# Optimization experiments

Hardware: AMD Instinct MI355X
Metric: run time of the kernel (lower is better)

Reference implementation:

```python
import jax, jax.numpy as jnp
import numpy as np

FEAT_STRIDE = 16
PRE_NMS = 6000   # TEST config
POST_NMS = 300
NMS_TH = 0.7


def _generate_anchors_3d(base_size=16, ratios=(0.5, 1.0, 2.0), scales=(8, 16, 32), time_dims=(16,)):
    """Standard Faster-RCNN anchor enumeration, extended with a time extent.
    Returns (A, 6) float32 boxes in [x1, y1, z1, x2, y2, z2] order (matches shift order)."""
    w = h = float(base_size)
    xc = yc = 0.5 * (base_size - 1)
    size = w * h
    ratios = np.asarray(ratios, dtype=np.float64)
    ws = np.round(np.sqrt(size / ratios))
    hs = np.round(ws * ratios)
    a2 = []
    for wi, hi in zip(ws, hs):
        for s in scales:
            ww, hh = wi * s, hi * s
            a2.append([xc - 0.5 * (ww - 1), yc - 0.5 * (hh - 1),
                       xc + 0.5 * (ww - 1), yc + 0.5 * (hh - 1)])
    out = []
    for t in time_dims:
        for a in a2:
            out.append([a[0], a[1], 0.0, a[2], a[3], float(t) - 1.0])
    return np.asarray(out, dtype=np.float32)


def setup_inputs() -> dict:
    key = jax.random.key(0)
    k1, k2 = jax.random.split(key)
    B, A, H, W, T = 2, 9, 32, 32, 16
    scores_map = jax.random.normal(k1, (B, 2 * A, H, W, T), dtype=jnp.float32)
    bbox_frame = jax.random.normal(k2, (B, 6 * A, H, W, T), dtype=jnp.float32) * 0.2
    im_info = jnp.array([512.0, 512.0, 16.0], dtype=jnp.float32)  # [img_h, img_w, n_frames]
    anchors = jnp.asarray(_generate_anchors_3d())  # (9, 6)
    return {"scores_map": scores_map, "bbox_frame": bbox_frame, "im_info": im_info, "anchors": anchors}


def _nms_single(boxes, scs):
    """Greedy 3D (spatio-temporal volume) NMS for one image.
    boxes: (N, 6), scs: (N,). Returns (POST_NMS, 7) rows [score, x1,y1,z1,x2,y2,z2],
    zero-padded past the number of kept proposals (matches output[i].zero_() + fill)."""
    order = jnp.argsort(-scs)[:PRE_NMS]           # descending score, pre-NMS top-k
    b = boxes[order]                              # (P, 6)
    s = scs[order]                                # (P,)
    vol = (b[:, 3] - b[:, 0] + 1.0) * (b[:, 4] - b[:, 1] + 1.0) * (b[:, 5] - b[:, 2] + 1.0)
    iw = jnp.clip(jnp.minimum(b[:, None, 3], b[None, :, 3]) - jnp.maximum(b[:, None, 0], b[None, :, 0]) + 1.0, 0.0)
    ih = jnp.clip(jnp.minimum(b[:, None, 4], b[None, :, 4]) - jnp.maximum(b[:, None, 1], b[None, :, 1]) + 1.0, 0.0)
    il = jnp.clip(jnp.minimum(b[:, None, 5], b[None, :, 5]) - jnp.maximum(b[:, None, 2], b[None, :, 2]) + 1.0, 0.0)
    inter = iw * ih * il                          # (P, P)
    iou = inter / (vol[:, None] + vol[None, :] - inter)
    iou = jax.lax.stop_gradient(iou)              # keep mask is non-differentiable
    P = b.shape[0]
    idx = jnp.arange(P)

    def step(keep, i):
        sup = (iou[i] > NMS_TH) & keep[i] & (idx > i)
        return keep & ~sup, None

    keep, _ = jax.lax.scan(step, jnp.ones((P,), dtype=bool), jnp.arange(P))
    rank = jnp.cumsum(keep) - 1
    pos = jnp.where(keep & (rank < POST_NMS), rank, POST_NMS)  # overflow slot POST_NMS
    rows = jnp.concatenate([s[:, None], b], axis=1)            # (P, 7)
    out = jnp.zeros((POST_NMS + 1, 7), dtype=boxes.dtype).at[pos].set(rows)
    return out[:POST_NMS]


def reference(scores_map, bbox_frame, im_info, anchors):
    A = anchors.shape[0]
    B = scores_map.shape[0]
    scores = scores_map[:, A:]                    # (B, A, H, W, T) foreground scores
    H, W, T = scores.shape[2], scores.shape[3], scores.shape[4]

    # --- anchor grid (matches np.meshgrid 'xy' + ravel = H-major, W, T order) ---
    sx = (jnp.arange(W) * FEAT_STRIDE).astype(scores_map.dtype)
    sy = (jnp.arange(H) * FEAT_STRIDE).astype(scores_map.dtype)
    sz = jnp.arange(T).astype(scores_map.dtype)
    X, Y, Z = jnp.meshgrid(sx, sy, sz)            # each (H, W, T)
    shift = jnp.stack([X.ravel(), Y.ravel(), Z.ravel()], axis=1)   # (K, 3)
    shifts = jnp.concatenate([shift, shift], axis=1)               # (K, 6)
    all_anchors = (anchors[None] + shifts[:, None]).reshape(-1, 6)  # (K*A, 6)

    deltas = bbox_frame.transpose(0, 2, 3, 4, 1).reshape(B, -1, 6)  # (B, K*A, 6)
    scs = scores.transpose(0, 2, 3, 4, 1).reshape(B, -1)            # (B, K*A)

    # --- bbox_transform_inv_3d ---
    aw = all_anchors[:, 3] - all_anchors[:, 0] + 1.0
    ah = all_anchors[:, 4] - all_anchors[:, 1] + 1.0
    al = all_anchors[:, 5] - all_anchors[:, 2] + 1.0
    acx = all_anchors[:, 0] + 0.5 * aw
    acy = all_anchors[:, 1] + 0.5 * ah
    acz = all_anchors[:, 2] + 0.5 * al
    pcx = deltas[..., 0] * aw + acx
    pcy = deltas[..., 1] * ah + acy
    pcz = deltas[..., 2] * al + acz
    pw = jnp.exp(deltas[..., 3]) * aw
    ph = jnp.exp(deltas[..., 4]) * ah
    pl = jnp.exp(deltas[..., 5]) * al
    proposals = jnp.stack([pcx - 0.5 * pw, pcy - 0.5 * ph, pcz - 0.5 * pl,
                           pcx + 0.5 * pw, pcy + 0.5 * ph, pcz + 0.5 * pl], axis=-1)

    # --- clip_boxes_3d: x in [0, img_w-1], y in [0, img_h-1], z in [0, n_frames-1] ---
    lim = jnp.stack([im_info[1], im_info[0], im_info[2],
                     im_info[1], im_info[0], im_info[2]]) - 1.0
    proposals = jnp.clip(proposals, 0.0, lim)

    return jax.vmap(_nms_single)(proposals, scs)  # (B, POST_NMS, 7)
```

## Files before the change

kernel.cpp:

```cpp
#include <hip/hip_runtime.h>
#include <stdint.h>

#define FEAT_STRIDE 16
#define PRE_NMS 6000
#define POST_NMS 300
#define NMS_TH 0.7f

static constexpr int B_ = 2, A_ = 9, H_ = 32, W_ = 32, T_ = 16;
static constexpr int LOC = H_ * W_ * T_;
static constexpr int N_ = LOC * A_;
static constexpr int NBIN = 65536;
static constexpr int NREP = 8;
static constexpr int CAP = 8192;
static constexpr int NW = 94;
static constexpr int ROWS = 6016;

static constexpr double BMID = 0.7000000178813934326171875;


__device__ __forceinline__ uint32_t f2u(float f) {
    uint32_t b = __float_as_uint(f);
    return b ^ ((b >> 31) ? 0xFFFFFFFFu : 0x80000000u);
}
__device__ __forceinline__ float u2f(uint32_t u) {
    uint32_t b = (u >> 31) ? (u ^ 0x80000000u) : ~u;
    return __uint_as_float(b);
}
__device__ __forceinline__ unsigned long long rl64(unsigned long long v, int lane) {
    unsigned int lo = (unsigned int)__builtin_amdgcn_readlane((int)(unsigned int)v, lane);
    unsigned int hi = (unsigned int)__builtin_amdgcn_readlane((int)(unsigned int)(v >> 32), lane);
    return ((unsigned long long)hi << 32) | lo;
}

__global__ void hist_kernel(const float* __restrict__ scores_map,
                            unsigned int* __restrict__ histR) {
    int gid = blockIdx.x * blockDim.x + threadIdx.x;
    if (gid >= B_ * N_) return;
    int b = gid / N_;
    int r = gid - b * N_;
    int a = r / LOC;
    int loc = r - a * LOC;
    float sc = scores_map[((size_t)(b * 2 * A_ + A_ + a)) * LOC + loc];
    uint32_t u = f2u(sc);
    int rep = blockIdx.x & (NREP - 1);
    atomicAdd(&histR[((size_t)(rep * B_ + b)) * NBIN + (u >> 16)], 1u);
}

__global__ void __launch_bounds__(256) partial_kernel(
        const unsigned int* __restrict__ histR,
        unsigned int* __restrict__ partials) {
    int c = blockIdx.x, bb = blockIdx.y, t = threadIdx.x;
    unsigned int s = 0;
#pragma unroll
    for (int r = 0; r < NREP; ++r) {
        const uint4* h4 = reinterpret_cast<const uint4*>(
            histR + ((size_t)(r * B_ + bb)) * NBIN + c * 1024);
        uint4 v = h4[t];
        s += v.x + v.y + v.z + v.w;
    }
    __shared__ unsigned int red[256];
    red[t] = s;
    __syncthreads();
    for (int off = 128; off > 0; off >>= 1) {
        if (t < off) red[t] += red[t + off];
        __syncthreads();
    }
    if (t == 0) partials[bb * 64 + c] = red[0];
}

__global__ void __launch_bounds__(256) rewrite_kernel(
        const unsigned int* __restrict__ histR,
        unsigned int* __restrict__ hist,
        unsigned int* __restrict__ binbase,
        const unsigned int* __restrict__ partials,
        unsigned int* __restrict__ thr) {
    int c = blockIdx.x, bb = blockIdx.y, t = threadIdx.x;
    __shared__ unsigned int sp[64];
    __shared__ unsigned int ssum[256];
    if (t < 64) sp[t] = partials[bb * 64 + t];
    uint4 v = {0u, 0u, 0u, 0u};
#pragma unroll
    for (int r = 0; r < NREP; ++r) {
        const uint4* h4 = reinterpret_cast<const uint4*>(
            histR + ((size_t)(r * B_ + bb)) * NBIN + c * 1024);
        uint4 w = h4[t];
        v.x += w.x; v.y += w.y; v.z += w.z; v.w += w.w;
    }
    unsigned int* h = hist + (size_t)bb * NBIN + c * 1024;
    unsigned int* bs = binbase + (size_t)bb * NBIN + c * 1024;
    ssum[t] = v.x + v.y + v.z + v.w;
    __syncthreads();
    unsigned int chunkBase = 0;
    for (int q = c + 1; q < 64; ++q) chunkBase += sp[q];
    for (int off = 1; off < 256; off <<= 1) {
        unsigned int val = (t + off < 256) ? ssum[t + off] : 0u;
        __syncthreads();
        ssum[t] += val;
        __syncthreads();
    }
    unsigned int run = chunkBase + ((t < 255) ? ssum[t + 1] : 0u);
    unsigned int cnt[4] = {v.x, v.y, v.z, v.w};
    unsigned int offv[4];
    for (int q = 3; q >= 0; --q) {
        offv[q] = run;
        unsigned int newrun = run + cnt[q];
        if (run < (unsigned)PRE_NMS && newrun >= (unsigned)PRE_NMS) {
            thr[bb * 2 + 0] = (unsigned)(c * 1024 + t * 4 + q);
            thr[bb * 2 + 1] = newrun;
        }
        run = newrun;
    }
    uint4 o4 = {offv[0], offv[1], offv[2], offv[3]};
    reinterpret_cast<uint4*>(h)[t] = o4;
    reinterpret_cast<uint4*>(bs)[t] = o4;
}

__global__ void __launch_bounds__(256) compact_kernel(
        const float* __restrict__ scores_map,
        const unsigned int* __restrict__ thr,
        unsigned long long* __restrict__ cand,
        unsigned int* __restrict__ hist) {
    int tid = threadIdx.x;
    int gid = blockIdx.x * 256 + tid;
    int b = gid / N_;
    int r = gid - b * N_;
    int a = r / LOC;
    int loc = r - a * LOC;
    float sc = scores_map[((size_t)(b * 2 * A_ + A_ + a)) * LOC + loc];
    uint32_t u = f2u(sc);
    uint32_t bin = u >> 16;
    if (bin >= thr[b * 2]) {
        int n = loc * A_ + a;
        unsigned long long key = ((unsigned long long)u << 18)
                               | (unsigned long long)(N_ - 1 - n);
        unsigned int slot = atomicAdd(&hist[b * NBIN + bin], 1u);
        if (slot < (unsigned)CAP)
            cand[(size_t)b * CAP + slot] = key;
    }
}

__global__ void __launch_bounds__(256) bucket_decode(
        const unsigned long long* __restrict__ cand,
        const unsigned int* __restrict__ hist,
        const unsigned int* __restrict__ binbase,
        const unsigned int* __restrict__ thr,
        const float* __restrict__ bbox_frame,
        const float* __restrict__ im_info,
        const float* __restrict__ anchors,
        float* __restrict__ sortedBox) {
    int gid = blockIdx.x * 256 + threadIdx.x;
    int bb = gid / CAP;
    int i = gid - bb * CAP;
    int count = (int)thr[bb * 2 + 1];
    if (count > CAP) count = CAP;
    if (i >= count) return;
    const unsigned long long* cb = cand + (size_t)bb * CAP;
    unsigned long long me = cb[i];
    int bin = (int)(me >> 34);
    int start = (int)binbase[bb * NBIN + bin];
    int end = (int)hist[bb * NBIN + bin];
    if (end > count) end = count;
    int rank = start;
    for (int q = start; q < end; ++q)
        rank += (cb[q] > me);
    if (rank >= PRE_NMS) return;

    uint32_t u = (uint32_t)(me >> 18);
    int n = N_ - 1 - (int)(me & 0x3FFFFull);
    int a = n % A_;
    int loc = n / A_;
    int k = loc % T_;
    int j = (loc / T_) % W_;
    int ii = loc / (T_ * W_);

    float ax1 = anchors[a * 6 + 0] + (float)(FEAT_STRIDE * j);
    float ay1 = anchors[a * 6 + 1] + (float)(FEAT_STRIDE * ii);
    float az1 = anchors[a * 6 + 2] + (float)k;
    float ax2 = anchors[a * 6 + 3] + (float)(FEAT_STRIDE * j);
    float ay2 = anchors[a * 6 + 4] + (float)(FEAT_STRIDE * ii);
    float az2 = anchors[a * 6 + 5] + (float)k;
    float aw = ax2 - ax1 + 1.0f, ah = ay2 - ay1 + 1.0f, al = az2 - az1 + 1.0f;
    float acx = ax1 + 0.5f * aw, acy = ay1 + 0.5f * ah, acz = az1 + 0.5f * al;

    const float* dp = bbox_frame + ((size_t)(bb * 6 * A_ + a * 6)) * LOC
                    + ii * (W_ * T_) + j * T_ + k;
    float d0 = dp[0 * LOC], d1 = dp[1 * LOC], d2 = dp[2 * LOC];
    float d3 = dp[3 * LOC], d4 = dp[4 * LOC], d5 = dp[5 * LOC];

    float pcx = d0 * aw + acx, pcy = d1 * ah + acy, pcz = d2 * al + acz;
    float pw = expf(d3) * aw, ph = expf(d4) * ah, pl = expf(d5) * al;

    float x1 = pcx - 0.5f * pw, y1 = pcy - 0.5f * ph, z1 = pcz - 0.5f * pl;
    float x2 = pcx + 0.5f * pw, y2 = pcy + 0.5f * ph, z2 = pcz + 0.5f * pl;

    float lx = im_info[1] - 1.0f, ly = im_info[0] - 1.0f, lz = im_info[2] - 1.0f;
    x1 = fminf(fmaxf(x1, 0.0f), lx); y1 = fminf(fmaxf(y1, 0.0f), ly); z1 = fminf(fmaxf(z1, 0.0f), lz);
    x2 = fminf(fmaxf(x2, 0.0f), lx); y2 = fminf(fmaxf(y2, 0.0f), ly); z2 = fminf(fmaxf(z2, 0.0f), lz);

    float vol = (x2 - x1 + 1.0f) * (y2 - y1 + 1.0f) * (z2 - z1 + 1.0f);
    float* p = sortedBox + ((size_t)bb * ROWS + rank) * 8;
    p[0] = x1; p[1] = y1; p[2] = z1; p[3] = x2;
    p[4] = y2; p[5] = z2; p[6] = vol; p[7] = u2f(u);
}

__global__ void mask_build(const float* __restrict__ sortedBox,
                           unsigned long long* __restrict__ mask,
                           unsigned long long* __restrict__ band) {
    int g = blockIdx.x / NW, w = blockIdx.x % NW;
    if (w < g) return;
    int bb = blockIdx.y;
    int lane = threadIdx.x;
    __shared__ float4 colA[64];
    __shared__ float4 colB[64];
    const float* sb = sortedBox + (size_t)bb * ROWS * 8;
    int col = w * 64 + lane;
    if (col < PRE_NMS) {
        const float4* cp4 = reinterpret_cast<const float4*>(sb + (size_t)col * 8);
        float4 lo = cp4[0], hi = cp4[1];
        colA[lane] = make_float4(lo.x, lo.y, lo.z, lo.w);
        colB[lane] = make_float4(hi.x, hi.y, hi.z, 0.0f);
    } else {
        colA[lane] = make_float4(3e8f, 0.0f, 0.0f, -3e8f);
        colB[lane] = make_float4(0.0f, 0.0f, 1.0f, 0.0f);
    }
    __syncthreads();
    int row = g * 64 + lane;
    if (row >= PRE_NMS) return;
    const float4* rp4 = reinterpret_cast<const float4*>(sb + (size_t)row * 8);
    float4 rlo = rp4[0], rhi = rp4[1];
    float x1 = rlo.x, y1 = rlo.y, z1 = rlo.z;
    float x2 = rlo.w, y2 = rhi.x, z2 = rhi.y, v = rhi.z;
    unsigned long long word = 0;
#pragma unroll 8
    for (int b2 = 0; b2 < 64; ++b2) {
        float4 cA = colA[b2];
        float4 cB = colB[b2];
        float iw = fminf(x2, cA.w) - fmaxf(x1, cA.x) + 1.0f;
        float ih = fminf(y2, cB.x) - fmaxf(y1, cA.y) + 1.0f;
        float il = fminf(z2, cB.y) - fmaxf(z1, cA.z) + 1.0f;
        iw = fmaxf(iw, 0.0f); ih = fmaxf(ih, 0.0f); il = fmaxf(il, 0.0f);
        float inter = iw * ih * il;
        float denom = v + cB.z - inter;
        bool over = ((double)inter >= BMID * (double)denom);
        int cidx = w * 64 + b2;
        if (cidx > row && over) word |= (1ull << b2);
    }
    mask[((size_t)bb * NW + w) * ROWS + row] = word;
    unsigned long long* bd = band + ((size_t)bb * ROWS + row) * 4;
    if (w == g) {
        bd[0] = word;
        if (g + 1 >= NW) bd[1] = 0ull;
        if (g + 2 >= NW) bd[2] = 0ull;
    }
    if (w == g + 1) bd[1] = word;
    if (w == g + 2) bd[2] = word;
}

__global__ void __launch_bounds__(1024) suppress_kernel(
        const unsigned long long* __restrict__ mask,
        const unsigned long long* __restrict__ band,
        const float* __restrict__ sortedBox,
        float* __restrict__ out) {
    int bb = blockIdx.x;
    int tid = threadIdx.x;
    int lane = tid & 63;
    __shared__ unsigned long long remv[NW];
    __shared__ int kr[3][64];
    __shared__ int keptAll[POST_NMS];
    __shared__ int snk[3];
    __shared__ int stot[2];
    for (int i = tid; i < NW; i += 1024) remv[i] = 0ull;
    if (tid == 0) {
        remv[NW - 1] = ~((1ull << (PRE_NMS - (NW - 1) * 64)) - 1ull);
        snk[0] = snk[1] = snk[2] = 0;
    }
    __syncthreads();

    const unsigned long long* M  = mask + (size_t)bb * NW * ROWS;
    const unsigned long long* Bd = band + (size_t)bb * ROWS * 4;
    const float* sb = sortedBox + (size_t)bb * ROWS * 8;
    float* ob = out + (size_t)bb * POST_NMS * 7;

    unsigned long long d0 = 0, d1 = 0, d2 = 0;
    unsigned long long supCur = 0, S1 = 0, S2 = 0;
    unsigned long long pend[8];
    int kept_total = 0;
    if (tid < 64) {
        const ulonglong2* bp = reinterpret_cast<const ulonglong2*>(&Bd[(size_t)lane * 4]);
        ulonglong2 v01 = bp[0], v23 = bp[1];
        d0 = v01.x; d1 = v01.y; d2 = v23.x;
    }

    int total = 0;
    for (int c = 0; c < NW; ++c) {
        if (tid < 64) {
            unsigned long long n0 = 0, n1 = 0, n2 = 0;
            if (c + 1 < NW) {
                const ulonglong2* bp = reinterpret_cast<const ulonglong2*>(
                    &Bd[(size_t)((c + 1) * 64 + lane) * 4]);
                ulonglong2 v01 = bp[0], v23 = bp[1];
                n0 = v01.x; n1 = v01.y; n2 = v23.x;
            }
            unsigned long long alive = ~(remv[c] | supCur);
            int nk = 0;
            while (alive && kept_total + nk < POST_NMS) {
                int b = (int)__builtin_ctzll(alive);
                int bs = __builtin_amdgcn_readfirstlane(b);
                unsigned long long dr = rl64(d0, bs);
                if (lane == 0) {
                    kr[c % 3][nk] = c * 64 + bs;
                    keptAll[kept_total + nk] = c * 64 + bs;
                }
                S1 |= rl64(d1, bs);
                S2 |= rl64(d2, bs);
                ++nk;
                alive &= ~(dr | (1ull << bs));
            }
            kept_total += nk;
            if (lane == 0) { snk[c % 3] = nk; stot[c & 1] = kept_total; }
            supCur = S1; S1 = S2; S2 = 0;
            d0 = n0; d1 = n1; d2 = n2;
        } else {
            int t = tid - 64;
            int wi = t >> 3, s = t & 7;
            if (c >= 2) {
                int t2 = c - 2;
                int w = t2 + 3 + wi;
                int nk2 = snk[t2 % 3];
                if (w < NW && s < nk2) {
                    unsigned long long acc = 0;
#pragma unroll
                    for (int q = 0; q < 8; ++q) {
                        int i = s + q * 8;
                        if (i < nk2) acc |= pend[q];
                    }
                    atomicOr(&remv[w], acc);
                }
            }
            if (c >= 1) {
                int t1 = c - 1;
                int w = t1 + 3 + wi;
                int nk1 = snk[t1 % 3];
                if (w < NW) {
#pragma unroll
                    for (int q = 0; q < 8; ++q) {
                        int i = s + q * 8;
                        if (i < nk1) pend[q] = M[(size_t)w * ROWS + kr[t1 % 3][i]];
                    }
                }
            }
        }
        asm volatile("s_waitcnt lgkmcnt(0)" ::: "memory");
        __builtin_amdgcn_s_barrier();
        asm volatile("" ::: "memory");
        total = stot[c & 1];
        if (total >= POST_NMS) break;
    }

    for (int e = tid; e < total * 7; e += 1024) {
        int i = e / 7, j = e - i * 7;
        ob[e] = sb[(size_t)keptAll[i] * 8 + (j == 0 ? 7 : j - 1)];
    }
    for (int idx = total * 7 + tid; idx < POST_NMS * 7; idx += 1024)
        ob[idx] = 0.0f;
}

extern "C" void kernel_launch(void* const* d_in, const int* in_sizes, int n_in,
                              void* d_out, int out_size, void* d_ws, size_t ws_size,
                              hipStream_t stream) {
    const float* scores_map = (const float*)d_in[0];
    const float* bbox_frame = (const float*)d_in[1];
    const float* im_info    = (const float*)d_in[2];
    const float* anchors    = (const float*)d_in[3];
    float* out = (float*)d_out;

    char* ws = (char*)d_ws;
    unsigned long long* mask  = (unsigned long long*)(ws + 0);
    unsigned int* binbase     = (unsigned int*)(ws + 0);
    unsigned int* histR       = (unsigned int*)(ws + 524288);
    float* sortedBox          = (float*)(ws + 9048064);
    unsigned long long* cand  = (unsigned long long*)(ws + 9433088);
    unsigned int* hist        = (unsigned int*)(ws + 9564160);
    unsigned long long* band  = (unsigned long long*)(ws + 9564160);
    unsigned int* thr         = (unsigned int*)(ws + 10088448);
    unsigned int* partials    = (unsigned int*)(ws + 10088464);

    hipMemsetAsync(histR, 0, (size_t)NREP * B_ * NBIN * 4, stream);

    int total = B_ * N_;
    hist_kernel<<<(total + 255) / 256, 256, 0, stream>>>(scores_map, histR);
    partial_kernel<<<dim3(64, B_), 256, 0, stream>>>(histR, partials);
    rewrite_kernel<<<dim3(64, B_), 256, 0, stream>>>(histR, hist, binbase, partials, thr);
    compact_kernel<<<total / 256, 256, 0, stream>>>(scores_map, thr, cand, hist);
    bucket_decode<<<B_ * CAP / 256, 256, 0, stream>>>(cand, hist, binbase, thr,
                                                      bbox_frame, im_info, anchors,
                                                      sortedBox);
    mask_build<<<dim3(NW * NW, B_), 64, 0, stream>>>(sortedBox, mask, band);
    suppress_kernel<<<B_, 1024, 0, stream>>>(mask, band, sortedBox, out);
}
```

Measured before the change: 138.6 us.

## Widen NMS suppression band to three words and double-buffer pending mask loads

The in-register band of precomputed suppression words is widened from two to three following 64-box chunks, so the leader wave handles more near-diagonal suppression itself. The global mask loads issued by the helper waves get two cycles of latency before being ORed into the shared remove bitmap, using two pending buffers and a loop unrolled by two. This aims to hide global-load latency in the serial chunk loop, at the cost of an extra band word per row, more registers, and an extra readlane per kept box.

```diff
diff --git a/kernel.cpp b/kernel.cpp
--- a/kernel.cpp
+++ b/kernel.cpp
@@ -251,9 +251,11 @@
         bd[0] = word;
         if (g + 1 >= NW) bd[1] = 0ull;
         if (g + 2 >= NW) bd[2] = 0ull;
+        if (g + 3 >= NW) bd[3] = 0ull;
     }
     if (w == g + 1) bd[1] = word;
     if (w == g + 2) bd[2] = word;
+    if (w == g + 3) bd[3] = word;
 }
 
 __global__ void __launch_bounds__(1024) suppress_kernel(
@@ -265,14 +267,15 @@
     int tid = threadIdx.x;
     int lane = tid & 63;
     __shared__ unsigned long long remv[NW];
-    __shared__ int kr[3][64];
+    __shared__ int kr[4][64];
     __shared__ int keptAll[POST_NMS];
-    __shared__ int snk[3];
+    __shared__ int snk[4];
     __shared__ int stot[2];
     for (int i = tid; i < NW; i += 1024) remv[i] = 0ull;
     if (tid == 0) {
         remv[NW - 1] = ~((1ull << (PRE_NMS - (NW - 1) * 64)) - 1ull);
-        snk[0] = snk[1] = snk[2] = 0;
+        snk[0] = snk[1] = snk[2] = snk[3] = 0;
+        stot[0] = stot[1] = 0;
     }
     __syncthreads();
 
@@ -281,81 +284,93 @@
     const float* sb = sortedBox + (size_t)bb * ROWS * 8;
     float* ob = out + (size_t)bb * POST_NMS * 7;
 
-    unsigned long long d0 = 0, d1 = 0, d2 = 0;
-    unsigned long long supCur = 0, S1 = 0, S2 = 0;
-    unsigned long long pend[8];
+    unsigned long long d0 = 0, d1 = 0, d2 = 0, d3 = 0;
+    unsigned long long supCur = 0, S1 = 0, S2 = 0, S3 = 0;
+    unsigned long long pendA[8], pendB[8];
     int kept_total = 0;
+    int total = 0;
+    bool stop = false;
     if (tid < 64) {
         const ulonglong2* bp = reinterpret_cast<const ulonglong2*>(&Bd[(size_t)lane * 4]);
         ulonglong2 v01 = bp[0], v23 = bp[1];
-        d0 = v01.x; d1 = v01.y; d2 = v23.x;
-    }
-
-    int total = 0;
-    for (int c = 0; c < NW; ++c) {
-        if (tid < 64) {
-            unsigned long long n0 = 0, n1 = 0, n2 = 0;
-            if (c + 1 < NW) {
-                const ulonglong2* bp = reinterpret_cast<const ulonglong2*>(
-                    &Bd[(size_t)((c + 1) * 64 + lane) * 4]);
-                ulonglong2 v01 = bp[0], v23 = bp[1];
-                n0 = v01.x; n1 = v01.y; n2 = v23.x;
-            }
-            unsigned long long alive = ~(remv[c] | supCur);
-            int nk = 0;
-            while (alive && kept_total + nk < POST_NMS) {
-                int b = (int)__builtin_ctzll(alive);
-                int bs = __builtin_amdgcn_readfirstlane(b);
-                unsigned long long dr = rl64(d0, bs);
-                if (lane == 0) {
-                    kr[c % 3][nk] = c * 64 + bs;
-                    keptAll[kept_total + nk] = c * 64 + bs;
-                }
-                S1 |= rl64(d1, bs);
-                S2 |= rl64(d2, bs);
-                ++nk;
-                alive &= ~(dr | (1ull << bs));
-            }
-            kept_total += nk;
-            if (lane == 0) { snk[c % 3] = nk; stot[c & 1] = kept_total; }
-            supCur = S1; S1 = S2; S2 = 0;
-            d0 = n0; d1 = n1; d2 = n2;
-        } else {
-            int t = tid - 64;
-            int wi = t >> 3, s = t & 7;
-            if (c >= 2) {
-                int t2 = c - 2;
-                int w = t2 + 3 + wi;
-                int nk2 = snk[t2 % 3];
-                if (w < NW && s < nk2) {
-                    unsigned long long acc = 0;
-#pragma unroll
-                    for (int q = 0; q < 8; ++q) {
-                        int i = s + q * 8;
-                        if (i < nk2) acc |= pend[q];
-                    }
-                    atomicOr(&remv[w], acc);
-                }
-            }
-            if (c >= 1) {
-                int t1 = c - 1;
-                int w = t1 + 3 + wi;
-                int nk1 = snk[t1 % 3];
-                if (w < NW) {
-#pragma unroll
-                    for (int q = 0; q < 8; ++q) {
-                        int i = s + q * 8;
-                        if (i < nk1) pend[q] = M[(size_t)w * ROWS + kr[t1 % 3][i]];
-                    }
-                }
-            }
+        d0 = v01.x; d1 = v01.y; d2 = v23.x; d3 = v23.y;
+    }
+
+#define SUP_STEP(CVAL, PEND)                                                     \
+    {                                                                            \
+        const int c = (CVAL);                                                    \
+        if (tid < 64) {                                                          \
+            unsigned long long n0 = 0, n1 = 0, n2 = 0, n3 = 0;                   \
+            if (c + 1 < NW) {                                                    \
+                const ulonglong2* bp = reinterpret_cast<const ulonglong2*>(      \
+                    &Bd[(size_t)((c + 1) * 64 + lane) * 4]);                     \
+                ulonglong2 v01 = bp[0], v23 = bp[1];                             \
+                n0 = v01.x; n1 = v01.y; n2 = v23.x; n3 = v23.y;                  \
+            }                                                                    \
+            unsigned long long alive = ~(remv[c] | supCur);                      \
+            int nk = 0;                                                          \
+            while (alive && kept_total + nk < POST_NMS) {                        \
+                int b_ = (int)__builtin_ctzll(alive);                            \
+                int bs = __builtin_amdgcn_readfirstlane(b_);                     \
+                unsigned long long dr = rl64(d0, bs);                            \
+                if (lane == 0) {                                                 \
+                    kr[c & 3][nk] = c * 64 + bs;                                 \
+                    keptAll[kept_total + nk] = c * 64 + bs;                      \
+                }                                                                \
+                S1 |= rl64(d1, bs);                                              \
+                S2 |= rl64(d2, bs);                                              \
+                S3 |= rl64(d3, bs);                                              \
+                ++nk;                                                            \
+                alive &= ~(dr | (1ull << bs));                                   \
+            }                                                                    \
+            kept_total += nk;                                                    \
+            if (lane == 0) { snk[c & 3] = nk; stot[c & 1] = kept_total; }        \
+            supCur = S1; S1 = S2; S2 = S3; S3 = 0;                               \
+            d0 = n0; d1 = n1; d2 = n2; d3 = n3;                                  \
+        } else {                                                                 \
+            int t = tid - 64;                                                    \
+            int wi = t >> 3, s = t & 7;                                          \
+            if (c >= 3) {                                \
+                int k = c - 3;                                                   \
+                int w = k + 4 + wi;                                              \
+                int nk2 = snk[k & 3];                                            \
+                if (w < NW && nk2 > 0) {                                         \
+                    unsigned long long acc = 0;                                  \
+                    _Pragma("unroll")                                            \
+                    for (int q = 0; q < 8; ++q) {                                \
+                        int i = s + q * 8;                                       \
+                        if (i < nk2) acc |= PEND[q];                             \
+                    }                                                            \
+                    if (acc) atomicOr(&remv[w], acc);                            \
+                }                                                                \
+            }                                                                    \
+            if (c >= 1) {                        \
+                int k = c - 1;                                                   \
+                int w = k + 4 + wi;                                              \
+                int nk1 = snk[k & 3];                                            \
+                if (w < NW) {                                                    \
+                    _Pragma("unroll")                                            \
+                    for (int q = 0; q < 8; ++q) {                                \
+                        int i = s + q * 8;                                       \
+                        if (i < nk1) PEND[q] = M[(size_t)w * ROWS + kr[k & 3][i]]; \
+                    }                                                            \
+                }                                                                \
+            }                                                                    \
+        }                                                                        \
+        asm volatile("s_waitcnt lgkmcnt(0)" ::: "memory");                       \
+        __builtin_amdgcn_s_barrier();                                            \
+        asm volatile("" ::: "memory");                                           \
+        total = stot[c & 1];                                                     \
+        if (total >= POST_NMS) stop = true;                                      \
+    }
+
+    for (int cc = 0; cc < NW && !stop; cc += 2) {
+        SUP_STEP(cc, pendB);
+        if (!stop) {
+            SUP_STEP(cc + 1, pendA);
         }
-        asm volatile("s_waitcnt lgkmcnt(0)" ::: "memory");
-        __builtin_amdgcn_s_barrier();
-        asm volatile("" ::: "memory");
-        total = stot[c & 1];
-        if (total >= POST_NMS) break;
-    }
+    }
+#undef SUP_STEP
 
     for (int e = tid; e < total * 7; e += 1024) {
         int i = e / 7, j = e - i * 7;
```

After: 141.7 us. +2.3%, slower.

## Replace barrier-stepped NMS suppression with flag-synchronized producer/consumer waves

Applied to the files above, without the earlier changes.

The suppress kernel moves from a 1024-thread block that hits a block-wide barrier every 64-box chunk to 256 threads. One scanner wave walks the chunks and publishes progress through an LDS flag. Three consumer waves round-robin the chunks, load mask rows and atomically OR them into the shared remove mask, each signalling completion with its own flag. The band now carries a fourth diagonal word so the scanner can run further ahead of the consumers. The aim is to take per-chunk barrier latency off the serial critical path. In exchange it adds spin-wait polling on shared memory and fewer threads to issue the mask-row loads.

```diff
diff --git a/kernel.cpp b/kernel.cpp
--- a/kernel.cpp
+++ b/kernel.cpp
@@ -251,28 +251,35 @@
         bd[0] = word;
         if (g + 1 >= NW) bd[1] = 0ull;
         if (g + 2 >= NW) bd[2] = 0ull;
+        if (g + 3 >= NW) bd[3] = 0ull;
     }
     if (w == g + 1) bd[1] = word;
     if (w == g + 2) bd[2] = word;
-}
-
-__global__ void __launch_bounds__(1024) suppress_kernel(
+    if (w == g + 3) bd[3] = word;
+}
+
+__global__ void __launch_bounds__(256) suppress_kernel(
         const unsigned long long* __restrict__ mask,
         const unsigned long long* __restrict__ band,
         const float* __restrict__ sortedBox,
         float* __restrict__ out) {
     int bb = blockIdx.x;
     int tid = threadIdx.x;
-    int lane = tid & 63;
+    int lane = tid & 63, wv = tid >> 6;
     __shared__ unsigned long long remv[NW];
-    __shared__ int kr[3][64];
+    __shared__ int kr[8][64];
     __shared__ int keptAll[POST_NMS];
-    __shared__ int snk[3];
-    __shared__ int stot[2];
-    for (int i = tid; i < NW; i += 1024) remv[i] = 0ull;
+    __shared__ int snk[8];
+    __shared__ int scanned;
+    __shared__ int applied[3];
+    __shared__ int stopf;
+    __shared__ int stotal;
+    for (int i = tid; i < NW; i += 256) remv[i] = 0ull;
     if (tid == 0) {
         remv[NW - 1] = ~((1ull << (PRE_NMS - (NW - 1) * 64)) - 1ull);
-        snk[0] = snk[1] = snk[2] = 0;
+        scanned = 0; stopf = 0; stotal = 0;
+        applied[0] = 0; applied[1] = 1; applied[2] = 2;
+        for (int q = 0; q < 8; ++q) snk[q] = 0;
     }
     __syncthreads();
 
@@ -281,87 +288,143 @@
     const float* sb = sortedBox + (size_t)bb * ROWS * 8;
     float* ob = out + (size_t)bb * POST_NMS * 7;
 
-    unsigned long long d0 = 0, d1 = 0, d2 = 0;
-    unsigned long long supCur = 0, S1 = 0, S2 = 0;
-    unsigned long long pend[8];
-    int kept_total = 0;
-    if (tid < 64) {
-        const ulonglong2* bp = reinterpret_cast<const ulonglong2*>(&Bd[(size_t)lane * 4]);
-        ulonglong2 v01 = bp[0], v23 = bp[1];
-        d0 = v01.x; d1 = v01.y; d2 = v23.x;
-    }
-
-    int total = 0;
-    for (int c = 0; c < NW; ++c) {
-        if (tid < 64) {
-            unsigned long long n0 = 0, n1 = 0, n2 = 0;
-            if (c + 1 < NW) {
-                const ulonglong2* bp = reinterpret_cast<const ulonglong2*>(
-                    &Bd[(size_t)((c + 1) * 64 + lane) * 4]);
-                ulonglong2 v01 = bp[0], v23 = bp[1];
-                n0 = v01.x; n1 = v01.y; n2 = v23.x;
+    if (wv == 0) {
+        unsigned long long a0, a1, a2, a3, b0, b1, b2, b3;
+        {
+            const ulonglong2* bp = reinterpret_cast<const ulonglong2*>(&Bd[(size_t)lane * 4]);
+            ulonglong2 v01 = bp[0], v23 = bp[1];
+            a0 = v01.x; a1 = v01.y; a2 = v23.x; a3 = v23.y;
+        }
+        {
+            const ulonglong2* bp = reinterpret_cast<const ulonglong2*>(&Bd[(size_t)(64 + lane) * 4]);
+            ulonglong2 v01 = bp[0], v23 = bp[1];
+            b0 = v01.x; b1 = v01.y; b2 = v23.x; b3 = v23.y;
+        }
+        unsigned long long supCur = 0, S1 = 0, S2 = 0, S3 = 0;
+        int kept_total = 0;
+        bool stop = false;
+
+#define SUP_STEP(CVAL, D0, D1, D2, D3)                                          \
+        {                                                                       \
+            const int c = (CVAL);                                               \
+            if (c >= 4) {                                                       \
+                while (true) {                                                  \
+                    int x0 = __hip_atomic_load(&applied[0], __ATOMIC_RELAXED,   \
+                                               __HIP_MEMORY_SCOPE_WORKGROUP);   \
+                    int x1 = __hip_atomic_load(&applied[1], __ATOMIC_RELAXED,   \
+                                               __HIP_MEMORY_SCOPE_WORKGROUP);   \
+                    int x2 = __hip_atomic_load(&applied[2], __ATOMIC_RELAXED,   \
+                                               __HIP_MEMORY_SCOPE_WORKGROUP);   \
+                    if (x0 > c - 4 && x1 > c - 4 && x2 > c - 4) break;          \
+                    __builtin_amdgcn_s_sleep(1);                                \
+                }                                                               \
+                __threadfence_block();                                          \
+            }                                                                   \
+            unsigned long long alive = ~(remv[c] | supCur);                     \
+            int nk = 0;                                                         \
+            while (alive && kept_total + nk < POST_NMS) {                       \
+                int b_ = (int)__builtin_ctzll(alive);                           \
+                int bs = __builtin_amdgcn_readfirstlane(b_);                    \
+                unsigned long long dr = rl64(D0, bs);                           \
+                if (lane == 0) {                                                \
+                    kr[c & 7][nk] = c * 64 + bs;                                \
+                    keptAll[kept_total + nk] = c * 64 + bs;                     \
+                }                                                               \
+                S1 |= rl64(D1, bs);                                             \
+                S2 |= rl64(D2, bs);                                             \
+                S3 |= rl64(D3, bs);                                             \
+                ++nk;                                                           \
+                alive &= ~(dr | (1ull << bs));                                  \
+            }                                                                   \
+            kept_total += nk;                                                   \
+            if (lane == 0) {                                                    \
+                snk[c & 7] = nk;                                                \
+                __hip_atomic_store(&scanned, c + 1, __ATOMIC_RELEASE,           \
+                                   __HIP_MEMORY_SCOPE_WORKGROUP);               \
+            }                                                                   \
+            supCur = S1; S1 = S2; S2 = S3; S3 = 0;                              \
+            if (kept_total >= POST_NMS) {                                       \
+                stop = true;                                                    \
+            } else if (c + 2 < NW) {                                            \
+                const ulonglong2* bp = reinterpret_cast<const ulonglong2*>(     \
+                    &Bd[(size_t)((c + 2) * 64 + lane) * 4]);                    \
+                ulonglong2 v01 = bp[0], v23 = bp[1];                            \
+                D0 = v01.x; D1 = v01.y; D2 = v23.x; D3 = v23.y;                 \
+            }                                                                   \
+        }
+
+        for (int cc = 0; cc < NW && !stop; cc += 2) {
+            SUP_STEP(cc, a0, a1, a2, a3);
+            if (!stop) {
+                SUP_STEP(cc + 1, b0, b1, b2, b3);
             }
-            unsigned long long alive = ~(remv[c] | supCur);
-            int nk = 0;
-            while (alive && kept_total + nk < POST_NMS) {
-                int b = (int)__builtin_ctzll(alive);
-                int bs = __builtin_amdgcn_readfirstlane(b);
-                unsigned long long dr = rl64(d0, bs);
-                if (lane == 0) {
-                    kr[c % 3][nk] = c * 64 + bs;
-                    keptAll[kept_total + nk] = c * 64 + bs;
+        }
+#undef SUP_STEP
+        if (lane == 0) {
+            stotal = kept_total;
+            __hip_atomic_store(&stopf, 1, __ATOMIC_RELEASE,
+                               __HIP_MEMORY_SCOPE_WORKGROUP);
+        }
+    } else {
+        int gw = wv - 1;
+        for (int k = gw; k < NW; k += 3) {
+            bool bail = false;
+            while (true) {
+                int s = __hip_atomic_load(&scanned, __ATOMIC_ACQUIRE,
+                                          __HIP_MEMORY_SCOPE_WORKGROUP);
+                if (s > k) break;
+                if (__hip_atomic_load(&stopf, __ATOMIC_RELAXED,
+                                      __HIP_MEMORY_SCOPE_WORKGROUP)) { bail = true; break; }
+                __builtin_amdgcn_s_sleep(1);
+            }
+            if (bail) break;
+            int nk = snk[k & 7];
+            int W = NW - (k + 4);
+            if (nk > 0 && W > 0) {
+                int w0 = k + 4 + lane;
+                int w1 = w0 + 64;
+                bool g0 = lane < W, g1 = lane + 64 < W;
+                unsigned long long acc0 = 0, acc1 = 0;
+                for (int ib = 0; ib < nk; ib += 4) {
+                    int r0 = kr[k & 7][ib];
+                    int r1 = (ib + 1 < nk) ? kr[k & 7][ib + 1] : -1;
+                    int r2 = (ib + 2 < nk) ? kr[k & 7][ib + 2] : -1;
+                    int r3 = (ib + 3 < nk) ? kr[k & 7][ib + 3] : -1;
+                    unsigned long long pa0 = 0, pa1 = 0, pb0 = 0, pb1 = 0;
+                    unsigned long long pc0 = 0, pc1 = 0, pd0 = 0, pd1 = 0;
+                    if (g0) pa0 = M[(size_t)w0 * ROWS + r0];
+                    if (g1) pa1 = M[(size_t)w1 * ROWS + r0];
+                    if (r1 >= 0) {
+                        if (g0) pb0 = M[(size_t)w0 * ROWS + r1];
+                        if (g1) pb1 = M[(size_t)w1 * ROWS + r1];
+                    }
+                    if (r2 >= 0) {
+                        if (g0) pc0 = M[(size_t)w0 * ROWS + r2];
+                        if (g1) pc1 = M[(size_t)w1 * ROWS + r2];
+                    }
+                    if (r3 >= 0) {
+                        if (g0) pd0 = M[(size_t)w0 * ROWS + r3];
+                        if (g1) pd1 = M[(size_t)w1 * ROWS + r3];
+                    }
+                    acc0 |= pa0 | pb0 | pc0 | pd0;
+                    acc1 |= pa1 | pb1 | pc1 | pd1;
                 }
-                S1 |= rl64(d1, bs);
-                S2 |= rl64(d2, bs);
-                ++nk;
-                alive &= ~(dr | (1ull << bs));
+                if (g0 && acc0) atomicOr(&remv[w0], acc0);
+                if (g1 && acc1) atomicOr(&remv[w1], acc1);
             }
-            kept_total += nk;
-            if (lane == 0) { snk[c % 3] = nk; stot[c & 1] = kept_total; }
-            supCur = S1; S1 = S2; S2 = 0;
-            d0 = n0; d1 = n1; d2 = n2;
-        } else {
-            int t = tid - 64;
-            int wi = t >> 3, s = t & 7;
-            if (c >= 2) {
-                int t2 = c - 2;
-                int w = t2 + 3 + wi;
-                int nk2 = snk[t2 % 3];
-                if (w < NW && s < nk2) {
-                    unsigned long long acc = 0;
-#pragma unroll
-                    for (int q = 0; q < 8; ++q) {
-                        int i = s + q * 8;
-                        if (i < nk2) acc |= pend[q];
-                    }
-                    atomicOr(&remv[w], acc);
-                }
-            }
-            if (c >= 1) {
-                int t1 = c - 1;
-                int w = t1 + 3 + wi;
-                int nk1 = snk[t1 % 3];
-                if (w < NW) {
-#pragma unroll
-                    for (int q = 0; q < 8; ++q) {
-                        int i = s + q * 8;
-                        if (i < nk1) pend[q] = M[(size_t)w * ROWS + kr[t1 % 3][i]];
-                    }
-                }
-            }
-        }
-        asm volatile("s_waitcnt lgkmcnt(0)" ::: "memory");
-        __builtin_amdgcn_s_barrier();
-        asm volatile("" ::: "memory");
-        total = stot[c & 1];
-        if (total >= POST_NMS) break;
-    }
-
-    for (int e = tid; e < total * 7; e += 1024) {
+            __threadfence_block();
+            __hip_atomic_store(&applied[gw], k + 3, __ATOMIC_RELEASE,
+                               __HIP_MEMORY_SCOPE_WORKGROUP);
+        }
+    }
+    __syncthreads();
+
+    int total = stotal;
+    for (int e = tid; e < total * 7; e += 256) {
         int i = e / 7, j = e - i * 7;
         ob[e] = sb[(size_t)keptAll[i] * 8 + (j == 0 ? 7 : j - 1)];
     }
-    for (int idx = total * 7 + tid; idx < POST_NMS * 7; idx += 1024)
+    for (int idx = total * 7 + tid; idx < POST_NMS * 7; idx += 256)
         ob[idx] = 0.0f;
 }
 
@@ -396,5 +459,5 @@
                                                       bbox_frame, im_info, anchors,
                                                       sortedBox);
     mask_build<<<dim3(NW * NW, B_), 64, 0, stream>>>(sortedBox, mask, band);
-    suppress_kernel<<<B_, 1024, 0, stream>>>(mask, band, sortedBox, out);
-}
+    suppress_kernel<<<B_, 256, 0, stream>>>(mask, band, sortedBox, out);
+}
```

Result: no change. 139.7 us (+0.8%).

## Run NMS suppression in a single wavefront with register-resident removal bitmask

Applied to the files above, without the earlier changes.

Replaces the 1024-thread suppression kernel, which used a producer wave plus helper waves doing shared-memory atomics and a block barrier every chunk, with a single-wavefront loop. Each lane now holds two 64-bit removal words in registers and loads mask rows for kept boxes directly. Those loads are software-pipelined through a 4-deep pend buffer, and band rows are prefetched four chunks ahead. This removes per-chunk barriers and LDS atomics from the serial critical path, at the cost of one wave issuing all mask loads and higher register pressure. The band array now carries a fourth word, written by mask_build.

```diff
diff --git a/kernel.cpp b/kernel.cpp
--- a/kernel.cpp
+++ b/kernel.cpp
@@ -251,117 +251,146 @@
         bd[0] = word;
         if (g + 1 >= NW) bd[1] = 0ull;
         if (g + 2 >= NW) bd[2] = 0ull;
+        if (g + 3 >= NW) bd[3] = 0ull;
     }
     if (w == g + 1) bd[1] = word;
     if (w == g + 2) bd[2] = word;
-}
-
-__global__ void __launch_bounds__(1024) suppress_kernel(
+    if (w == g + 3) bd[3] = word;
+}
+
+__global__ void __launch_bounds__(256) suppress_kernel(
         const unsigned long long* __restrict__ mask,
         const unsigned long long* __restrict__ band,
         const float* __restrict__ sortedBox,
         float* __restrict__ out) {
     int bb = blockIdx.x;
     int tid = threadIdx.x;
-    int lane = tid & 63;
-    __shared__ unsigned long long remv[NW];
-    __shared__ int kr[3][64];
+    int lane = tid & 63, wv = tid >> 6;
     __shared__ int keptAll[POST_NMS];
-    __shared__ int snk[3];
-    __shared__ int stot[2];
-    for (int i = tid; i < NW; i += 1024) remv[i] = 0ull;
-    if (tid == 0) {
-        remv[NW - 1] = ~((1ull << (PRE_NMS - (NW - 1) * 64)) - 1ull);
-        snk[0] = snk[1] = snk[2] = 0;
-    }
-    __syncthreads();
+    __shared__ int stotal;
 
     const unsigned long long* M  = mask + (size_t)bb * NW * ROWS;
     const unsigned long long* Bd = band + (size_t)bb * ROWS * 4;
     const float* sb = sortedBox + (size_t)bb * ROWS * 8;
     float* ob = out + (size_t)bb * POST_NMS * 7;
 
-    unsigned long long d0 = 0, d1 = 0, d2 = 0;
-    unsigned long long supCur = 0, S1 = 0, S2 = 0;
-    unsigned long long pend[8];
-    int kept_total = 0;
-    if (tid < 64) {
-        const ulonglong2* bp = reinterpret_cast<const ulonglong2*>(&Bd[(size_t)lane * 4]);
-        ulonglong2 v01 = bp[0], v23 = bp[1];
-        d0 = v01.x; d1 = v01.y; d2 = v23.x;
-    }
-
-    int total = 0;
-    for (int c = 0; c < NW; ++c) {
-        if (tid < 64) {
-            unsigned long long n0 = 0, n1 = 0, n2 = 0;
-            if (c + 1 < NW) {
-                const ulonglong2* bp = reinterpret_cast<const ulonglong2*>(
-                    &Bd[(size_t)((c + 1) * 64 + lane) * 4]);
-                ulonglong2 v01 = bp[0], v23 = bp[1];
-                n0 = v01.x; n1 = v01.y; n2 = v23.x;
-            }
-            unsigned long long alive = ~(remv[c] | supCur);
-            int nk = 0;
-            while (alive && kept_total + nk < POST_NMS) {
-                int b = (int)__builtin_ctzll(alive);
-                int bs = __builtin_amdgcn_readfirstlane(b);
-                unsigned long long dr = rl64(d0, bs);
-                if (lane == 0) {
-                    kr[c % 3][nk] = c * 64 + bs;
-                    keptAll[kept_total + nk] = c * 64 + bs;
-                }
-                S1 |= rl64(d1, bs);
-                S2 |= rl64(d2, bs);
-                ++nk;
-                alive &= ~(dr | (1ull << bs));
-            }
-            kept_total += nk;
-            if (lane == 0) { snk[c % 3] = nk; stot[c & 1] = kept_total; }
-            supCur = S1; S1 = S2; S2 = 0;
-            d0 = n0; d1 = n1; d2 = n2;
-        } else {
-            int t = tid - 64;
-            int wi = t >> 3, s = t & 7;
-            if (c >= 2) {
-                int t2 = c - 2;
-                int w = t2 + 3 + wi;
-                int nk2 = snk[t2 % 3];
-                if (w < NW && s < nk2) {
-                    unsigned long long acc = 0;
+    if (wv == 0) {
+        const unsigned long long* rowp0 = M + (size_t)lane * ROWS;
+        int l1 = lane + 64; if (l1 > NW - 1) l1 = NW - 1;
+        const unsigned long long* rowp1 = M + (size_t)l1 * ROWS;
+
+        unsigned long long r0 = 0, r1 = 0;
+        if (lane == NW - 1 - 64)
+            r1 = ~((1ull << (PRE_NMS - (NW - 1) * 64)) - 1ull);
+
+        unsigned long long pend[4][8][2];
 #pragma unroll
-                    for (int q = 0; q < 8; ++q) {
-                        int i = s + q * 8;
-                        if (i < nk2) acc |= pend[q];
-                    }
-                    atomicOr(&remv[w], acc);
-                }
-            }
-            if (c >= 1) {
-                int t1 = c - 1;
-                int w = t1 + 3 + wi;
-                int nk1 = snk[t1 % 3];
-                if (w < NW) {
+        for (int q = 0; q < 4; ++q)
 #pragma unroll
-                    for (int q = 0; q < 8; ++q) {
-                        int i = s + q * 8;
-                        if (i < nk1) pend[q] = M[(size_t)w * ROWS + kr[t1 % 3][i]];
-                    }
-                }
-            }
+            for (int i = 0; i < 8; ++i) { pend[q][i][0] = 0; pend[q][i][1] = 0; }
+
+        unsigned long long bd0[3], bd1[3], bd2[3], bd3[3];
+#define BAND_LOAD(CH, BD)                                                      \
+        {   const ulonglong2* bp_ = reinterpret_cast<const ulonglong2*>(       \
+                &Bd[(size_t)((CH) * 64 + lane) * 4]);                          \
+            ulonglong2 va_ = bp_[0];                                           \
+            BD[0] = va_.x; BD[1] = va_.y;                                      \
+            BD[2] = Bd[(size_t)((CH) * 64 + lane) * 4 + 2]; }
+        BAND_LOAD(0, bd0)
+        BAND_LOAD(1, bd1)
+        BAND_LOAD(2, bd2)
+        BAND_LOAD(3, bd3)
+
+        unsigned long long supCur = 0, S1 = 0, S2 = 0;
+        int kt = 0;
+        bool stop = false;
+
+#define CHUNK_BODY(CVAL, P, BD)                                                \
+        if (!stop) {                                                          \
+            const int c = (CVAL);                                             \
+            {             \
+                unsigned long long a0 = 0, a1 = 0;                            \
+                _Pragma("unroll")                                              \
+                for (int i = 0; i < 8; ++i) {                                  \
+                    a0 |= pend[((P) + 1) & 3][i][0];                           \
+                    a1 |= pend[((P) + 1) & 3][i][1];                           \
+                }                                                              \
+                r0 |= a0; r1 |= a1;                                            \
+                _Pragma("unroll")                                              \
+                for (int i = 0; i < 8; ++i) {                                  \
+                    pend[((P) + 1) & 3][i][0] = 0;                             \
+                    pend[((P) + 1) & 3][i][1] = 0;                             \
+                }                                                              \
+            }                                                                  \
+            unsigned long long cur = (c < 64) ? rl64(r0, c) : rl64(r1, c - 64);\
+            unsigned long long alive = ~(cur | supCur);                        \
+            int nk = 0;                                                        \
+            _Pragma("unroll")                                                  \
+            for (int i = 0; i < 8; ++i) {                                      \
+                if (alive && kt + nk < POST_NMS) {                             \
+                    int b_ = (int)__builtin_ctzll(alive);                      \
+                    int bs = __builtin_amdgcn_readfirstlane(b_);               \
+                    int R = c * 64 + bs;                                       \
+                    if (lane == 0) keptAll[kt + nk] = R;                       \
+                    unsigned long long dr = rl64(BD[0], bs);                   \
+                    S1 |= rl64(BD[1], bs);                                     \
+                    S2 |= rl64(BD[2], bs);                                     \
+                    pend[(P)][i][0] = rowp0[R];                                \
+                    pend[(P)][i][1] = rowp1[R];                                \
+                    ++nk;                                                      \
+                    alive &= ~(dr | (1ull << bs));                             \
+                }                                                              \
+            }                                                                  \
+            kt += nk;                                                          \
+            while (alive && kt < POST_NMS) {         \
+                unsigned long long o00 = 0, o01 = 0, o10 = 0, o11 = 0,         \
+                                   o20 = 0, o21 = 0, o30 = 0, o31 = 0;         \
+                _Pragma("unroll")                                              \
+                for (int i = 0; i < 4; ++i) {                                  \
+                    if (alive && kt < POST_NMS) {                              \
+                        int b_ = (int)__builtin_ctzll(alive);                  \
+                        int bs = __builtin_amdgcn_readfirstlane(b_);           \
+                        int R = c * 64 + bs;                                   \
+                        if (lane == 0) keptAll[kt] = R;                        \
+                        unsigned long long dr = rl64(BD[0], bs);               \
+                        S1 |= rl64(BD[1], bs);                                 \
+                        S2 |= rl64(BD[2], bs);                                 \
+                        if (i == 0)      { o00 = rowp0[R]; o01 = rowp1[R]; }   \
+                        else if (i == 1) { o10 = rowp0[R]; o11 = rowp1[R]; }   \
+                        else if (i == 2) { o20 = rowp0[R]; o21 = rowp1[R]; }   \
+                        else             { o30 = rowp0[R]; o31 = rowp1[R]; }   \
+                        ++kt;                                                  \
+                        alive &= ~(dr | (1ull << bs));                         \
+                    }                                                          \
+                }                                                              \
+                r0 |= o00 | o10 | o20 | o30;                                   \
+                r1 |= o01 | o11 | o21 | o31;                                   \
+            }                                                                  \
+            if (kt >= POST_NMS) stop = true;                                   \
+            supCur = S1; S1 = S2; S2 = 0;                                      \
+            if (c + 4 < NW) BAND_LOAD(c + 4, BD)                               \
         }
-        asm volatile("s_waitcnt lgkmcnt(0)" ::: "memory");
-        __builtin_amdgcn_s_barrier();
-        asm volatile("" ::: "memory");
-        total = stot[c & 1];
-        if (total >= POST_NMS) break;
-    }
-
-    for (int e = tid; e < total * 7; e += 1024) {
+
+        for (int cb = 0; cb < 92; cb += 4) {
+            CHUNK_BODY(cb + 0, 0, bd0)
+            CHUNK_BODY(cb + 1, 1, bd1)
+            CHUNK_BODY(cb + 2, 2, bd2)
+            CHUNK_BODY(cb + 3, 3, bd3)
+        }
+        CHUNK_BODY(92, 0, bd0)
+        CHUNK_BODY(93, 1, bd1)
+#undef CHUNK_BODY
+#undef BAND_LOAD
+        if (lane == 0) stotal = kt;
+    }
+    __syncthreads();
+
+    int total = stotal;
+    for (int e = tid; e < total * 7; e += 256) {
         int i = e / 7, j = e - i * 7;
         ob[e] = sb[(size_t)keptAll[i] * 8 + (j == 0 ? 7 : j - 1)];
     }
-    for (int idx = total * 7 + tid; idx < POST_NMS * 7; idx += 1024)
+    for (int idx = total * 7 + tid; idx < POST_NMS * 7; idx += 256)
         ob[idx] = 0.0f;
 }
 
@@ -396,5 +425,5 @@
                                                       bbox_frame, im_info, anchors,
                                                       sortedBox);
     mask_build<<<dim3(NW * NW, B_), 64, 0, stream>>>(sortedBox, mask, band);
-    suppress_kernel<<<B_, 1024, 0, stream>>>(mask, band, sortedBox, out);
-}
+    suppress_kernel<<<B_, 256, 0, stream>>>(mask, band, sortedBox, out);
+}
```

New measurement: 136.4 us. Within noise of the previous version (-1.6%).
